# Performance work log

Hardware: AMD Instinct MI355X
Metric: run time of the kernel (lower is better)

The kernel has to match this reference:

```python
import math
import jax, jax.numpy as jnp
import numpy as np

B, H, N, M, DQ, DV, P = 8, 16, 1024, 1024, 64, 64, 64
N_HEADS = 16


def setup_inputs() -> dict:
    key = jax.random.key(0)
    ks = jax.random.split(key, 6)
    return {
        "queries": jax.random.normal(ks[0], (B, H, N, DQ), dtype=jnp.float32),
        "keys": jax.random.normal(ks[1], (B, H, M, DQ), dtype=jnp.float32),
        "values": jax.random.normal(ks[2], (B, H, M, DV), dtype=jnp.float32),
        # learned relative positional encoding table, leading broadcast dim of 1
        "pos_enc": jax.random.normal(ks[3], (1, N, M, P), dtype=jnp.float32) * 0.02,
        # nn.Linear(P, 1): weight (1,P) stored flat as (P,), bias (1,)
        "w_pos": jax.random.normal(ks[4], (P,), dtype=jnp.float32) * (1.0 / math.sqrt(P)),
        "b_pos": jnp.zeros((1,), dtype=jnp.float32),
        "query_sequence_pad_length": N,
        "key_value_sequence_pad_length": M,
    }


def reference(queries, keys, values, pos_enc, w_pos, b_pos,
              query_sequence_pad_length, key_value_sequence_pad_length):
    n = query_sequence_pad_length
    m = key_value_sequence_pad_length
    Bsz, Hn = queries.shape[0], queries.shape[1]

    # source: tmp = keys if N == M else queries
    tmp = keys if queries.shape[2] == keys.shape[2] else queries
    # raw scores, scaled by 1/sqrt(n_heads) (faithful to source)
    scores = jnp.einsum('bhnd,bhmd->bhnm', tmp, keys) / math.sqrt(N_HEADS)  # (B,H,n,m)

    # map_pos(scores[...,None] + pos) with Linear(P,1) is affine, so it equals
    # scores * sum(w) + (pos . w + b)  — exact algebraic rewrite avoiding the
    # (B,H,n,m,P) broadcast blowup.
    pos_bias = jnp.einsum('nmp,p->nm', pos_enc[0, :n, :m, :], w_pos) + b_pos[0]  # (n,m)
    attn = scores * jnp.sum(w_pos) + pos_bias  # (B,H,n,m)

    attn = attn.reshape(Bsz * Hn, n, m)
    q = queries.reshape(Bsz * Hn, n, queries.shape[-1])
    k = keys.reshape(Bsz * Hn, m, keys.shape[-1])
    v = values.reshape(Bsz * Hn, m, values.shape[-1])
    return (attn, q, k, v)
```

## Files before the change

kernel.cpp:

```cpp
#include <hip/hip_runtime.h>
#include <hip/hip_bf16.h>

typedef __attribute__((ext_vector_type(8))) short short8;
typedef __attribute__((ext_vector_type(4))) float f32x4;
typedef unsigned int u32;

constexpr int N = 1024, M = 1024, D = 64, BH = 128;
constexpr size_t ATTN_ELEMS = (size_t)BH * N * M;
constexpr size_t QKV_ELEMS  = (size_t)BH * N * D;
constexpr int PB_BLOCKS = 2048;
constexpr int KCONV_BLOCKS = 512;
constexpr int COPY_BLOCKS_PER = 256;
constexpr int BGROUP = 8;
constexpr int BR = 32, BC = 256;

__device__ __forceinline__ short f2b(float x) {
    __hip_bfloat16 h = __float2bfloat16(x);
    return *reinterpret_cast<short*>(&h);
}

__device__ __forceinline__ void gl_lds16(const void* g, void* l) {
    __builtin_amdgcn_global_load_lds(
        (const __attribute__((address_space(1))) u32*)g,
        (__attribute__((address_space(3))) u32*)l, 16, 0, 0);
}

__global__ void prep_kernel(const float* __restrict__ q, const float* __restrict__ k,
                            const float* __restrict__ v, const float* __restrict__ pos,
                            const float* __restrict__ w, const float* __restrict__ b,
                            float* __restrict__ pb, short* __restrict__ kbf,
                            float* __restrict__ scale_p,
                            float* __restrict__ qout, float* __restrict__ kout,
                            float* __restrict__ vout, int ncopy) {
    const int bid = blockIdx.x, tid = threadIdx.x;
    if (bid < PB_BLOCKS) {
        const int lane16 = tid & 15;
        const f32x4 w4 = ((const f32x4*)w)[lane16];
        const float bias = b[0];
        const int group = (bid * 256 + tid) >> 4;
        const int ngroups = (PB_BLOCKS * 256) >> 4;
        for (int pair = group; pair < N * M; pair += ngroups) {
            f32x4 p = __builtin_nontemporal_load((const f32x4*)pos + (size_t)pair * 16 + lane16);
            float s = p[0]*w4[0] + p[1]*w4[1] + p[2]*w4[2] + p[3]*w4[3];
            s += __shfl_xor(s, 1);
            s += __shfl_xor(s, 2);
            s += __shfl_xor(s, 4);
            s += __shfl_xor(s, 8);
            if (lane16 == 0) pb[pair] = s + bias;
        }
    } else if (bid < PB_BLOCKS + KCONV_BLOCKS) {
        const int cid = bid - PB_BLOCKS;
        const int total_slots = BH * N * 8;
        for (int gs = cid * 256 + tid; gs < total_slots; gs += KCONV_BLOCKS * 256) {
            const int qs = gs & 7, gr = (gs >> 3) & (N - 1), bb = gs >> 13;
            const float* src = k + ((size_t)bb * N + gr) * D + (qs ^ (gr & 7)) * 8;
            f32x4 x0 = ((const f32x4*)src)[0], x1 = ((const f32x4*)src)[1];
            short8 pk;
#pragma unroll
            for (int e = 0; e < 4; e++) { pk[e] = f2b(x0[e]); pk[4 + e] = f2b(x1[e]); }
            *(short8*)&kbf[(size_t)gs * 8] = pk;
        }
    } else if (bid < PB_BLOCKS + KCONV_BLOCKS + ncopy) {
        const int cid = bid - PB_BLOCKS - KCONV_BLOCKS;
        const int which = cid >> 8, lid = cid & 255;
        const f32x4* __restrict__ src = (which == 0) ? (const f32x4*)q
                                      : (which == 1) ? (const f32x4*)k : (const f32x4*)v;
        f32x4* __restrict__ dst = (which == 0) ? (f32x4*)qout
                                : (which == 1) ? (f32x4*)kout : (f32x4*)vout;
        const int nel4 = (int)(QKV_ELEMS / 4);
        for (int i = lid * 256 + tid; i < nel4; i += COPY_BLOCKS_PER * 256) {
            f32x4 x = __builtin_nontemporal_load(src + i);
            __builtin_nontemporal_store(x, dst + i);
        }
    } else {
        if (tid < 64) {
            float val = w[tid];
#pragma unroll
            for (int o = 32; o > 0; o >>= 1) val += __shfl_down(val, o);
            if (tid == 0) scale_p[0] = val * 0.25f;
        }
    }
}

__launch_bounds__(256)
__global__ void attn_kernel(const short* __restrict__ kbf, const float* __restrict__ pb,
                            const float* __restrict__ scale_p, float* __restrict__ out) {
    __shared__ short lK[(BR + BC) * 64];
    const int pos = blockIdx.x;
    const int tr = pos >> 2, tc = pos & 3;
    const int batch0 = blockIdx.y * BGROUP;
    const int tid = threadIdx.x;
    const float scale = scale_p[0];

    const int lane = tid & 63, wv = tid >> 6;
    const int wr = wv >> 1, wc = wv & 1;
    const int frow = lane & 15;
    const int kslot = lane >> 4;

    const int orow = tr * BR + wr * 16 + (lane >> 4) * 4;
    const int ocol = tc * BC + wc * 128 + (lane & 15);

    f32x4 pf[8];
#pragma unroll
    for (int j = 0; j < 8; j++)
#pragma unroll
        for (int r = 0; r < 4; r++)
            pf[j][r] = pb[(size_t)(orow + r) * M + (ocol + j * 16)];

    for (int t = 0; t < BGROUP; ++t) {
        const short* __restrict__ Kb = kbf + (size_t)(batch0 + t) * N * 64;

#pragma unroll
        for (int it = 0; it < 9; ++it) {
            const int slot = it * 256 + tid;
            const int row = slot >> 3, qs = slot & 7;
            const int gr = (row < BR) ? (tr * BR + row) : (tc * BC + (row - BR));
            gl_lds16(Kb + (size_t)gr * 64 + qs * 8, &lK[slot * 8]);
        }
        __syncthreads();

        f32x4 acc[8] = {};
#pragma unroll
        for (int h = 0; h < 2; ++h) {
            const int ra = wr * 16 + frow;
            short8 a = *(const short8*)&lK[ra * 64 + ((h * 4 + kslot) ^ (ra & 7)) * 8];
#pragma unroll
            for (int j = 0; j < 8; j++) {
                const int rb = BR + wc * 128 + j * 16 + frow;
                short8 bf = *(const short8*)&lK[rb * 64 + ((h * 4 + kslot) ^ (rb & 7)) * 8];
                acc[j] = __builtin_amdgcn_mfma_f32_16x16x32_bf16(a, bf, acc[j], 0, 0, 0);
            }
        }

        const size_t obase = (size_t)(batch0 + t) * N * M;
#pragma unroll
        for (int j = 0; j < 8; j++)
#pragma unroll
            for (int r = 0; r < 4; r++) {
                out[obase + (size_t)(orow + r) * M + (ocol + j * 16)]
                    = acc[j][r] * scale + pf[j][r];
            }
        __syncthreads();
    }
}

extern "C" void kernel_launch(void* const* d_in, const int* in_sizes, int n_in,
                              void* d_out, int out_size, void* d_ws, size_t ws_size,
                              hipStream_t stream) {
    const float* queries = (const float*)d_in[0];
    const float* keys    = (const float*)d_in[1];
    const float* values  = (const float*)d_in[2];
    const float* pos_enc = (const float*)d_in[3];
    const float* w_pos   = (const float*)d_in[4];
    const float* b_pos   = (const float*)d_in[5];

    float* out  = (float*)d_out;
    float* qout = out + ATTN_ELEMS;
    float* kout = qout + QKV_ELEMS;
    float* vout = kout + QKV_ELEMS;

    const size_t need_ws = ((size_t)N * M + 16) * sizeof(float)
                         + (size_t)BH * N * 64 * sizeof(short);
    const int npos = (N / BR) * (M / BC);

    if (ws_size >= need_ws) {
        float* pb      = (float*)d_ws;
        float* scale_p = pb + (size_t)N * M;
        short* kbf     = (short*)(scale_p + 16);
        const int ncopy = 3 * COPY_BLOCKS_PER;
        prep_kernel<<<dim3(PB_BLOCKS + KCONV_BLOCKS + ncopy + 1), dim3(256), 0, stream>>>(
            queries, keys, values, pos_enc, w_pos, b_pos, pb, kbf, scale_p,
            qout, kout, vout, ncopy);
        attn_kernel<<<dim3(npos, BH / BGROUP), dim3(256), 0, stream>>>(kbf, pb, scale_p, out);
    } else {
        float* pb      = qout;
        float* scale_p = pb + (size_t)N * M;
        short* kbf     = (short*)(scale_p + 16);
        prep_kernel<<<dim3(PB_BLOCKS + KCONV_BLOCKS + 1), dim3(256), 0, stream>>>(
            queries, keys, values, pos_enc, w_pos, b_pos, pb, kbf, scale_p,
            qout, kout, vout, 0);
        attn_kernel<<<dim3(npos, BH / BGROUP), dim3(256), 0, stream>>>(kbf, pb, scale_p, out);
        hipMemcpyAsync(qout, queries, QKV_ELEMS * sizeof(float), hipMemcpyDeviceToDevice, stream);
        hipMemcpyAsync(kout, keys,    QKV_ELEMS * sizeof(float), hipMemcpyDeviceToDevice, stream);
        hipMemcpyAsync(vout, values,  QKV_ELEMS * sizeof(float), hipMemcpyDeviceToDevice, stream);
    }
}
```

Baseline: 206.2 us.

## Loop row tiles per batch with register-resident K fragments and double-buffered A

New measurement: 355.6 us. +72.5%, slower.

```diff
diff --git a/kernel.cpp b/kernel.cpp
--- a/kernel.cpp
+++ b/kernel.cpp
@@ -11,7 +11,6 @@
 constexpr int PB_BLOCKS = 2048;
 constexpr int KCONV_BLOCKS = 512;
 constexpr int COPY_BLOCKS_PER = 256;
-constexpr int BGROUP = 8;
 constexpr int BR = 32, BC = 256;
 
 __device__ __forceinline__ short f2b(float x) {
@@ -85,62 +84,72 @@
 __launch_bounds__(256)
 __global__ void attn_kernel(const short* __restrict__ kbf, const float* __restrict__ pb,
                             const float* __restrict__ scale_p, float* __restrict__ out) {
-    __shared__ short lK[(BR + BC) * 64];
-    const int pos = blockIdx.x;
-    const int tr = pos >> 2, tc = pos & 3;
-    const int batch0 = blockIdx.y * BGROUP;
+    __shared__ short lB[BC * 64];
+    __shared__ short lA[2][BR * 64];
+    const int tc = blockIdx.x & 3;
+    const int batch = blockIdx.x >> 2;
     const int tid = threadIdx.x;
     const float scale = scale_p[0];
+    const short* __restrict__ Kb = kbf + (size_t)batch * N * 64;
 
     const int lane = tid & 63, wv = tid >> 6;
     const int wr = wv >> 1, wc = wv & 1;
     const int frow = lane & 15;
     const int kslot = lane >> 4;
 
-    const int orow = tr * BR + wr * 16 + (lane >> 4) * 4;
+#pragma unroll
+    for (int it = 0; it < 8; ++it) {
+        const int slot = it * 256 + tid;
+        const int row = slot >> 3, qs = slot & 7;
+        gl_lds16(Kb + (size_t)(tc * BC + row) * 64 + qs * 8, &lB[slot * 8]);
+    }
+    {
+        const int row = tid >> 3, qs = tid & 7;
+        gl_lds16(Kb + (size_t)row * 64 + qs * 8, &lA[0][tid * 8]);
+    }
+    __syncthreads();
+
+    short8 bfrag[2][8];
+#pragma unroll
+    for (int h = 0; h < 2; ++h)
+#pragma unroll
+        for (int j = 0; j < 8; ++j) {
+            const int rb = wc * 128 + j * 16 + frow;
+            bfrag[h][j] = *(const short8*)&lB[rb * 64 + ((h * 4 + kslot) ^ (rb & 7)) * 8];
+        }
+
     const int ocol = tc * BC + wc * 128 + (lane & 15);
+    const size_t obase = (size_t)batch * N * M;
 
-    f32x4 pf[8];
-#pragma unroll
-    for (int j = 0; j < 8; j++)
-#pragma unroll
-        for (int r = 0; r < 4; r++)
-            pf[j][r] = pb[(size_t)(orow + r) * M + (ocol + j * 16)];
+    for (int tr = 0; tr < 32; ++tr) {
+        const int cur = tr & 1;
+        if (tr) __syncthreads();
+        if (tr + 1 < 32) {
+            const int row = tid >> 3, qs = tid & 7;
+            gl_lds16(Kb + (size_t)((tr + 1) * BR + row) * 64 + qs * 8,
+                     &lA[cur ^ 1][tid * 8]);
+        }
 
-    for (int t = 0; t < BGROUP; ++t) {
-        const short* __restrict__ Kb = kbf + (size_t)(batch0 + t) * N * 64;
-
-#pragma unroll
-        for (int it = 0; it < 9; ++it) {
-            const int slot = it * 256 + tid;
-            const int row = slot >> 3, qs = slot & 7;
-            const int gr = (row < BR) ? (tr * BR + row) : (tc * BC + (row - BR));
-            gl_lds16(Kb + (size_t)gr * 64 + qs * 8, &lK[slot * 8]);
-        }
-        __syncthreads();
+        const int ra = wr * 16 + frow;
+        short8 a0 = *(const short8*)&lA[cur][ra * 64 + ((kslot)     ^ (ra & 7)) * 8];
+        short8 a1 = *(const short8*)&lA[cur][ra * 64 + ((4 + kslot) ^ (ra & 7)) * 8];
 
         f32x4 acc[8] = {};
 #pragma unroll
-        for (int h = 0; h < 2; ++h) {
-            const int ra = wr * 16 + frow;
-            short8 a = *(const short8*)&lK[ra * 64 + ((h * 4 + kslot) ^ (ra & 7)) * 8];
+        for (int j = 0; j < 8; ++j)
+            acc[j] = __builtin_amdgcn_mfma_f32_16x16x32_bf16(a0, bfrag[0][j], acc[j], 0, 0, 0);
 #pragma unroll
-            for (int j = 0; j < 8; j++) {
-                const int rb = BR + wc * 128 + j * 16 + frow;
-                short8 bf = *(const short8*)&lK[rb * 64 + ((h * 4 + kslot) ^ (rb & 7)) * 8];
-                acc[j] = __builtin_amdgcn_mfma_f32_16x16x32_bf16(a, bf, acc[j], 0, 0, 0);
+        for (int j = 0; j < 8; ++j)
+            acc[j] = __builtin_amdgcn_mfma_f32_16x16x32_bf16(a1, bfrag[1][j], acc[j], 0, 0, 0);
+
+        const int orow = tr * BR + wr * 16 + (lane >> 4) * 4;
+#pragma unroll
+        for (int j = 0; j < 8; ++j)
+#pragma unroll
+            for (int r = 0; r < 4; ++r) {
+                const size_t off = (size_t)(orow + r) * M + (ocol + j * 16);
+                out[obase + off] = acc[j][r] * scale + pb[off];
             }
-        }
-
-        const size_t obase = (size_t)(batch0 + t) * N * M;
-#pragma unroll
-        for (int j = 0; j < 8; j++)
-#pragma unroll
-            for (int r = 0; r < 4; r++) {
-                out[obase + (size_t)(orow + r) * M + (ocol + j * 16)]
-                    = acc[j][r] * scale + pf[j][r];
-            }
-        __syncthreads();
     }
 }
 
@@ -161,7 +170,7 @@
 
     const size_t need_ws = ((size_t)N * M + 16) * sizeof(float)
                          + (size_t)BH * N * 64 * sizeof(short);
-    const int npos = (N / BR) * (M / BC);
+    const int nblocks = (M / BC) * BH;
 
     if (ws_size >= need_ws) {
         float* pb      = (float*)d_ws;
@@ -171,7 +180,7 @@
         prep_kernel<<<dim3(PB_BLOCKS + KCONV_BLOCKS + ncopy + 1), dim3(256), 0, stream>>>(
             queries, keys, values, pos_enc, w_pos, b_pos, pb, kbf, scale_p,
             qout, kout, vout, ncopy);
-        attn_kernel<<<dim3(npos, BH / BGROUP), dim3(256), 0, stream>>>(kbf, pb, scale_p, out);
+        attn_kernel<<<dim3(nblocks), dim3(256), 0, stream>>>(kbf, pb, scale_p, out);
     } else {
         float* pb      = qout;
         float* scale_p = pb + (size_t)N * M;
@@ -179,7 +188,7 @@
         prep_kernel<<<dim3(PB_BLOCKS + KCONV_BLOCKS + 1), dim3(256), 0, stream>>>(
             queries, keys, values, pos_enc, w_pos, b_pos, pb, kbf, scale_p,
             qout, kout, vout, 0);
-        attn_kernel<<<dim3(npos, BH / BGROUP), dim3(256), 0, stream>>>(kbf, pb, scale_p, out);
+        attn_kernel<<<dim3(nblocks), dim3(256), 0, stream>>>(kbf, pb, scale_p, out);
         hipMemcpyAsync(qout, queries, QKV_ELEMS * sizeof(float), hipMemcpyDeviceToDevice, stream);
         hipMemcpyAsync(kout, keys,    QKV_ELEMS * sizeof(float), hipMemcpyDeviceToDevice, stream);
         hipMemcpyAsync(vout, values,  QKV_ELEMS * sizeof(float), hipMemcpyDeviceToDevice, stream);
```

## Double-buffer K tiles in LDS and prefetch next batch during compute

Applied to the files above, without the earlier changes.

New measurement: 211.6 us. +2.6%, slower.

```diff
diff --git a/kernel.cpp b/kernel.cpp
--- a/kernel.cpp
+++ b/kernel.cpp
@@ -85,7 +85,7 @@
 __launch_bounds__(256)
 __global__ void attn_kernel(const short* __restrict__ kbf, const float* __restrict__ pb,
                             const float* __restrict__ scale_p, float* __restrict__ out) {
-    __shared__ short lK[(BR + BC) * 64];
+    __shared__ short lK[2][(BR + BC) * 64];
     const int pos = blockIdx.x;
     const int tr = pos >> 2, tc = pos & 3;
     const int batch0 = blockIdx.y * BGROUP;
@@ -107,40 +107,64 @@
         for (int r = 0; r < 4; r++)
             pf[j][r] = pb[(size_t)(orow + r) * M + (ocol + j * 16)];
 
+#pragma unroll
+    for (int it = 0; it < 9; ++it) {
+        const int slot = it * 256 + tid;
+        const int row = slot >> 3, qs = slot & 7;
+        const int gr = (row < BR) ? (tr * BR + row) : (tc * BC + (row - BR));
+        gl_lds16(kbf + ((size_t)batch0 * N + gr) * 64 + qs * 8, &lK[0][slot * 8]);
+    }
+
     for (int t = 0; t < BGROUP; ++t) {
-        const short* __restrict__ Kb = kbf + (size_t)(batch0 + t) * N * 64;
-
-#pragma unroll
-        for (int it = 0; it < 9; ++it) {
-            const int slot = it * 256 + tid;
-            const int row = slot >> 3, qs = slot & 7;
-            const int gr = (row < BR) ? (tr * BR + row) : (tc * BC + (row - BR));
-            gl_lds16(Kb + (size_t)gr * 64 + qs * 8, &lK[slot * 8]);
-        }
-        __syncthreads();
+        const int cur = t & 1;
+        if (t + 1 < BGROUP) {
+            const short* __restrict__ Kn = kbf + (size_t)(batch0 + t + 1) * N * 64;
+#pragma unroll
+            for (int it = 0; it < 9; ++it) {
+                const int slot = it * 256 + tid;
+                const int row = slot >> 3, qs = slot & 7;
+                const int gr = (row < BR) ? (tr * BR + row) : (tc * BC + (row - BR));
+                gl_lds16(Kn + (size_t)gr * 64 + qs * 8, &lK[cur ^ 1][slot * 8]);
+            }
+        }
+        if (t == 0)                 asm volatile("s_waitcnt vmcnt(9)"  ::: "memory");
+        else if (t + 1 < BGROUP)    asm volatile("s_waitcnt vmcnt(41)" ::: "memory");
+        else                        asm volatile("s_waitcnt vmcnt(32)" ::: "memory");
+        __builtin_amdgcn_s_barrier();
+        asm volatile("" ::: "memory");
+
+        const int ra = wr * 16 + frow;
+        short8 a0 = *(const short8*)&lK[cur][ra * 64 + ((kslot)     ^ (ra & 7)) * 8];
+        short8 a1 = *(const short8*)&lK[cur][ra * 64 + ((4 + kslot) ^ (ra & 7)) * 8];
 
         f32x4 acc[8] = {};
 #pragma unroll
-        for (int h = 0; h < 2; ++h) {
-            const int ra = wr * 16 + frow;
-            short8 a = *(const short8*)&lK[ra * 64 + ((h * 4 + kslot) ^ (ra & 7)) * 8];
-#pragma unroll
-            for (int j = 0; j < 8; j++) {
-                const int rb = BR + wc * 128 + j * 16 + frow;
-                short8 bf = *(const short8*)&lK[rb * 64 + ((h * 4 + kslot) ^ (rb & 7)) * 8];
-                acc[j] = __builtin_amdgcn_mfma_f32_16x16x32_bf16(a, bf, acc[j], 0, 0, 0);
-            }
+        for (int j = 0; j < 8; ++j) {
+            const int rb = BR + wc * 128 + j * 16 + frow;
+            short8 b0 = *(const short8*)&lK[cur][rb * 64 + ((kslot)     ^ (rb & 7)) * 8];
+            acc[j] = __builtin_amdgcn_mfma_f32_16x16x32_bf16(a0, b0, acc[j], 0, 0, 0);
+        }
+#pragma unroll
+        for (int j = 0; j < 8; ++j) {
+            const int rb = BR + wc * 128 + j * 16 + frow;
+            short8 b1 = *(const short8*)&lK[cur][rb * 64 + ((4 + kslot) ^ (rb & 7)) * 8];
+            acc[j] = __builtin_amdgcn_mfma_f32_16x16x32_bf16(a1, b1, acc[j], 0, 0, 0);
         }
 
         const size_t obase = (size_t)(batch0 + t) * N * M;
 #pragma unroll
-        for (int j = 0; j < 8; j++)
-#pragma unroll
-            for (int r = 0; r < 4; r++) {
+        for (int j = 0; j < 8; ++j)
+#pragma unroll
+            for (int r = 0; r < 4; ++r) {
                 out[obase + (size_t)(orow + r) * M + (ocol + j * 16)]
                     = acc[j][r] * scale + pf[j][r];
             }
-        __syncthreads();
+
+        if (t + 1 < BGROUP) {
+            asm volatile("s_waitcnt lgkmcnt(0)" ::: "memory");
+            __builtin_amdgcn_s_barrier();
+            asm volatile("" ::: "memory");
+        }
     }
 }
 
```
